# Optimization experiments

Measured on AMD Instinct MI355X. Metric: run time of the kernel, lower is better.

## Reference

```python
import jax, jax.numpy as jnp
import numpy as np

N = 50000       # num_nodes
R = 8           # num_relations
H = 64          # hidden_channels
C = 16          # num_classes
E = 1_600_000   # num edges (avg degree 32)
T = 8192        # number of 'author' target nodes (first T nodes after to_homogeneous)


def setup_inputs() -> dict:
    key = jax.random.key(0)
    ks = jax.random.split(key, 12)
    s = 0.02
    return {
        "edge_index": jax.random.randint(ks[0], (2, E), 0, N),
        "edge_type": jax.random.randint(ks[1], (E,), 0, R),
        "num_target": T,
        # conv1 (featureless: weight is an embedding table [R, N, H], root is [N, H])
        "weight1": jax.random.normal(ks[2], (R, N, H), jnp.float32) * s,
        "root1": jax.random.normal(ks[3], (N, H), jnp.float32) * s,
        "bias1": jnp.zeros((H,), jnp.float32),
        # conv2
        "weight2": jax.random.normal(ks[4], (R, H, H), jnp.float32) * s,
        "root2": jax.random.normal(ks[5], (H, H), jnp.float32) * s,
        "bias2": jnp.zeros((H,), jnp.float32),
        # linear head
        "lin_w": jax.random.normal(ks[6], (H, C), jnp.float32) * s,
        "lin_b": jnp.zeros((C,), jnp.float32),
    }


def reference(edge_index, edge_type, num_target, weight1, root1, bias1,
              weight2, root2, bias2, lin_w, lin_b):
    src, dst = edge_index[0], edge_index[1]
    E_ = src.shape[0]

    # PyG RGCNConv aggregates with MEAN per relation, then sums over relations.
    # Count edges per (dst node, relation) to form the per-relation mean denominator.
    seg = dst * R + edge_type                          # [E] combined (node, relation) id
    cnt = jax.ops.segment_sum(jnp.ones((E_,), jnp.float32), seg, num_segments=N * R)
    scale = (1.0 / jnp.maximum(cnt, 1.0))[seg]         # [E]

    # ---- conv1: x is None -> message = weight1[edge_type][src] (embedding lookup) ----
    m1 = weight1[edge_type, src] * scale[:, None]      # [E, H]
    h1 = jax.ops.segment_sum(m1, dst, num_segments=N)  # [N, H]
    h1 = h1 + root1 + bias1                            # root1[arange(N)] == root1
    h1 = jax.nn.elu(h1)

    # ---- conv2: message = h1[src] @ weight2[edge_type] ----
    # Precompute per-relation node transforms [R, N, H], then gather per edge.
    hr = jnp.einsum('nh,rhk->rnk', h1, weight2)        # [R, N, H]
    m2 = hr[edge_type, src] * scale[:, None]           # [E, H]
    h2 = jax.ops.segment_sum(m2, dst, num_segments=N)  # [N, H]
    h2 = h2 + h1 @ root2 + bias2
    h2 = jax.nn.elu(h2)

    # ---- linear head on the target ('author') node slice ----
    out = h2[:num_target] @ lin_w + lin_b              # [T, C]
    return out
```

## Files before the change

### kernel.cpp

```cpp
#include <hip/hip_runtime.h>

#define NNODES 50000
#define NREL   8
#define HID    64
#define NCLS   16
#define NEDGE  1600000
#define NTGT   8192
#define HALF   4096
#define NBINS  (NNODES * NREL)
#define CHUNK  1024
#define NCHUNK ((NBINS + CHUNK - 1) / CHUNK)

__device__ __forceinline__ float elu1(float x) { return x > 0.f ? x : expm1f(x); }

__device__ __forceinline__ int pack_rec(int src, int rel, int cnt) {
  return src | (rel << 16) | (cnt << 19);
}

__device__ __forceinline__ unsigned long long ld_stat(unsigned long long* p) {
  return __hip_atomic_load(p, __ATOMIC_RELAXED, __HIP_MEMORY_SCOPE_AGENT);
}
__device__ __forceinline__ void st_stat(unsigned long long* p, unsigned long long v) {
  __hip_atomic_store(p, v, __ATOMIC_RELAXED, __HIP_MEMORY_SCOPE_AGENT);
}

__global__ void count_kernel(const int* __restrict__ ei, const int* __restrict__ et,
                             int* __restrict__ cnt, int* __restrict__ epos,
                             unsigned long long* __restrict__ status) {
  int gt = blockIdx.x * blockDim.x + threadIdx.x;
  if (gt < NCHUNK) status[gt] = 0;
  int e4 = gt * 4;
  if (e4 >= NEDGE) return;
  int4 d = *(const int4*)(ei + NEDGE + e4);
  int4 r = *(const int4*)(et + e4);
  int4 p;
  p.x = atomicAdd(&cnt[d.x * NREL + r.x], 1);
  p.y = atomicAdd(&cnt[d.y * NREL + r.y], 1);
  p.z = atomicAdd(&cnt[d.z * NREL + r.z], 1);
  p.w = atomicAdd(&cnt[d.w * NREL + r.w], 1);
  *(int4*)(epos + e4) = p;
}

__global__ __launch_bounds__(256) void scan_lb_kernel(
    const int* __restrict__ cnt, unsigned long long* __restrict__ status,
    int* __restrict__ binptr) {
  __shared__ int sw[4];
  __shared__ int srun;
  __shared__ int sbase;
  int t = threadIdx.x, lane = t & 63, wid = t >> 6;
  int c = blockIdx.x;
  int i = c * CHUNK + t * 4;
  int4 cv = make_int4(0, 0, 0, 0);
  if (i < NBINS) cv = *(const int4*)(cnt + i);
  int p0 = cv.x, p1 = p0 + cv.y, p2 = p1 + cv.z, s = p2 + cv.w;
  int v = s;
#pragma unroll
  for (int off = 1; off < 64; off <<= 1) {
    int u = __shfl_up(v, off);
    if (lane >= off) v += u;
  }
  if (lane == 63) sw[wid] = v;
  __syncthreads();
  if (t == 0) {
    int run = 0;
#pragma unroll
    for (int j = 0; j < 4; ++j) { int x = sw[j]; sw[j] = run; run += x; }
    srun = run;
    unsigned long long f = (c == 0) ? 2ull : 1ull;
    st_stat(&status[c], (f << 62) | (unsigned)run);
    if (c == 0) sbase = 0;
  }
  __syncthreads();
  if (c > 0 && t < 64) {
    long long tot = 0;
    int back = c - 1;
    for (;;) {
      int idx = back - lane;
      unsigned long long st = (2ull << 62);
      if (idx >= 0) st = ld_stat(&status[idx]);
      int flag = (int)(st >> 62);
      bool isinc = (idx < 0) || (flag == 2);
      bool isval = (idx < 0) || (flag >= 1);
      unsigned long long incb = __ballot(isinc);
      unsigned long long valb = __ballot(isval);
      unsigned long long notval = ~valb;
      int firstinv = notval ? (__ffsll((long long)notval) - 1) : 64;
      int firstinc = incb ? (__ffsll((long long)incb) - 1) : 64;
      if (firstinc < firstinv) {
        int val = (lane <= firstinc) ? (int)(st & 0xFFFFFFFFu) : 0;
#pragma unroll
        for (int off = 32; off >= 1; off >>= 1) val += __shfl_xor(val, off);
        tot += val;
        break;
      } else if (firstinv > 0) {
        int val = (lane < firstinv) ? (int)(st & 0xFFFFFFFFu) : 0;
#pragma unroll
        for (int off = 32; off >= 1; off >>= 1) val += __shfl_xor(val, off);
        tot += val;
        back -= firstinv;
      } else {
        __builtin_amdgcn_s_sleep(2);
      }
    }
    if (lane == 0) {
      sbase = (int)tot;
      st_stat(&status[c], (2ull << 62) | (unsigned)((int)tot + srun));
    }
  }
  __syncthreads();
  int base = sbase;
  if (i < NBINS) {
    int excl = base + sw[wid] + (v - s);
    *(int4*)(binptr + i) = make_int4(excl, excl + p0, excl + p1, excl + p2);
  }
  if (c == 0 && t == 0) binptr[NBINS] = NEDGE;
}

__global__ void scatter_kernel(const int* __restrict__ ei, const int* __restrict__ et,
                               const int* __restrict__ epos, const int* __restrict__ binptr,
                               int* __restrict__ epo) {
  int e4 = (blockIdx.x * blockDim.x + threadIdx.x) * 4;
  if (e4 >= NEDGE) return;
  int4 sv = *(const int4*)(ei + e4);
  int4 dv = *(const int4*)(ei + NEDGE + e4);
  int4 rv = *(const int4*)(et + e4);
  int4 pv = *(const int4*)(epos + e4);
  int srcs[4] = {sv.x, sv.y, sv.z, sv.w};
  int dsts[4] = {dv.x, dv.y, dv.z, dv.w};
  int rels[4] = {rv.x, rv.y, rv.z, rv.w};
  int poss[4] = {pv.x, pv.y, pv.z, pv.w};
#pragma unroll
  for (int j = 0; j < 4; ++j) {
    int bin = dsts[j] * NREL + rels[j];
    int b = binptr[bin];
    int c = binptr[bin + 1] - b;
    epo[b + poss[j]] = pack_rec(srcs[j], rels[j], c);
  }
}

__global__ __launch_bounds__(256) void conv1_kernel(
    const int* __restrict__ binptr, const int* __restrict__ epo,
    const float* __restrict__ w1, const float* __restrict__ root1,
    const float* __restrict__ bias1, float* __restrict__ h1) {
  int wave = blockIdx.x * 4 + (threadIdx.x >> 6);
  if (wave >= NNODES) return;
  int lane = threadIdx.x & 63;
  int g = lane >> 4;
  int col = (lane & 15) << 2;
  int b0 = binptr[wave * NREL], b8 = binptr[wave * NREL + NREL];
  float4 acc = make_float4(0.f, 0.f, 0.f, 0.f);
  for (int eb = b0; eb < b8; eb += 64) {
    int mb = min(64, b8 - eb);
    int q = epo[eb + min(lane, mb - 1)];
    for (int j = 0; j < mb; j += 32) {
      float4 a[8]; float sc[8];
#pragma unroll
      for (int u = 0; u < 8; ++u) {
        int e0 = j + u * 4;
        if (e0 < mb) {
          int ei = e0 + g;
          int eic = min(ei, mb - 1);
          int rec = __shfl(q, eic);
          int src = rec & 0xFFFF;
          int rel = (rec >> 16) & 7;
          int cnt = ((unsigned)rec) >> 19;
          float s = 1.0f / (float)cnt;
          sc[u] = (ei < mb) ? s : 0.f;
          a[u] = *(const float4*)(w1 + (((size_t)(unsigned)(rel * NNODES + src)) << 6) + col);
        } else {
          sc[u] = 0.f;
          a[u] = make_float4(0.f, 0.f, 0.f, 0.f);
        }
      }
#pragma unroll
      for (int u = 0; u < 8; ++u) {
        acc.x = fmaf(a[u].x, sc[u], acc.x);
        acc.y = fmaf(a[u].y, sc[u], acc.y);
        acc.z = fmaf(a[u].z, sc[u], acc.z);
        acc.w = fmaf(a[u].w, sc[u], acc.w);
      }
    }
  }
#pragma unroll
  for (int off = 16; off < 64; off <<= 1) {
    acc.x += __shfl_xor(acc.x, off);
    acc.y += __shfl_xor(acc.y, off);
    acc.z += __shfl_xor(acc.z, off);
    acc.w += __shfl_xor(acc.w, off);
  }
  if (g == 0) {
    float4 r = *(const float4*)(root1 + (((size_t)wave) << 6) + col);
    float4 bz = *(const float4*)(bias1 + col);
    float4 v;
    v.x = elu1(acc.x + r.x + bz.x);
    v.y = elu1(acc.y + r.y + bz.y);
    v.z = elu1(acc.z + r.z + bz.z);
    v.w = elu1(acc.w + r.w + bz.w);
    *(float4*)(h1 + (((size_t)wave) << 6) + col) = v;
  }
}

__global__ __launch_bounds__(256) void conv2a_kernel(
    const int* __restrict__ binptr, const int* __restrict__ epo,
    const float* __restrict__ h1, float* __restrict__ agg, int nodeBase, int nloc) {
  int wv = blockIdx.x * 4 + (threadIdx.x >> 6);
  if (wv >= nloc * NREL) return;
  int lane = threadIdx.x & 63;
  int g = lane >> 4;
  int col = (lane & 15) << 2;
  int r = wv & 7;
  int bin = (nodeBase + (wv >> 3)) * NREL + r;
  int bb = binptr[bin], ee = binptr[bin + 1];
  float4 s = make_float4(0.f, 0.f, 0.f, 0.f);
  for (int e = bb; e < ee; e += 64) {
    int mb = min(64, ee - e);
    int q = epo[e + min(lane, mb - 1)];
    for (int j = 0; j < mb; j += 16) {
      float4 a[4]; float vld[4];
#pragma unroll
      for (int u = 0; u < 4; ++u) {
        int e0 = j + u * 4;
        if (e0 < mb) {
          int ei = e0 + g;
          int eic = min(ei, mb - 1);
          int src = __shfl(q, eic) & 0xFFFF;
          vld[u] = (ei < mb) ? 1.f : 0.f;
          a[u] = *(const float4*)(h1 + (((size_t)(unsigned)src) << 6) + col);
        } else {
          vld[u] = 0.f;
          a[u] = make_float4(0.f, 0.f, 0.f, 0.f);
        }
      }
#pragma unroll
      for (int u = 0; u < 4; ++u) {
        s.x = fmaf(a[u].x, vld[u], s.x);
        s.y = fmaf(a[u].y, vld[u], s.y);
        s.z = fmaf(a[u].z, vld[u], s.z);
        s.w = fmaf(a[u].w, vld[u], s.w);
      }
    }
  }
#pragma unroll
  for (int off = 16; off < 64; off <<= 1) {
    s.x += __shfl_xor(s.x, off);
    s.y += __shfl_xor(s.y, off);
    s.z += __shfl_xor(s.z, off);
    s.w += __shfl_xor(s.w, off);
  }
  if (g == 0) {
    float scl = (ee > bb) ? 1.0f / (float)(ee - bb) : 0.f;
    *(float4*)(agg + (((size_t)wv) << 6) + col) =
        make_float4(s.x * scl, s.y * scl, s.z * scl, s.w * scl);
  }
}

__global__ __launch_bounds__(256, 4) void conv2b_kernel(
    const float* __restrict__ agg, const float* __restrict__ h1,
    const float* __restrict__ w2, const float* __restrict__ root2,
    const float* __restrict__ bias2, const float* __restrict__ lin_w,
    const float* __restrict__ lin_b, float* __restrict__ out, int nodeBase) {
  __shared__ float sW[HID * HID];
  int t = threadIdx.x, lane = t & 63, wid = t >> 6;
  int ln0 = blockIdx.x * 8 + wid * 2;
  float bz = bias2[lane];
  float o0 = bz, o1 = bz;
  for (int r = 0; r < NREL; ++r) {
    if (r) __syncthreads();
#pragma unroll
    for (int i = 0; i < 4; ++i)
      *(float4*)(sW + t * 4 + i * 1024) = *(const float4*)(w2 + (r << 12) + t * 4 + i * 1024);
    __syncthreads();
    const float* a0 = agg + (((size_t)((ln0 + 0) * NREL + r)) << 6);
    const float* a1 = agg + (((size_t)((ln0 + 1) * NREL + r)) << 6);
#pragma unroll 16
    for (int k = 0; k < HID; ++k) {
      float w = sW[(k << 6) + lane];
      o0 = fmaf(a0[k], w, o0);
      o1 = fmaf(a1[k], w, o1);
    }
  }
  __syncthreads();
#pragma unroll
  for (int i = 0; i < 4; ++i)
    *(float4*)(sW + t * 4 + i * 1024) = *(const float4*)(root2 + t * 4 + i * 1024);
  __syncthreads();
  int g0 = nodeBase + ln0;
  const float* r0p = h1 + ((size_t)(g0 + 0) << 6);
  const float* r1p = h1 + ((size_t)(g0 + 1) << 6);
#pragma unroll 16
  for (int k = 0; k < HID; ++k) {
    float w = sW[(k << 6) + lane];
    o0 = fmaf(r0p[k], w, o0);
    o1 = fmaf(r1p[k], w, o1);
  }
  __syncthreads();
  int row0 = wid * 2;
  sW[row0 * 65 + lane] = elu1(o0);
  sW[(row0 + 1) * 65 + lane] = elu1(o1);
  float* lw = sW + 8 * 65;
  *(float4*)(lw + t * 4) = *(const float4*)(lin_w + t * 4);
  __syncthreads();
  if (t < 8 * NCLS) {
    int n = t >> 4, c = t & 15;
    float accv = lin_b[c];
#pragma unroll 16
    for (int l = 0; l < HID; ++l)
      accv = fmaf(sW[n * 65 + l], lw[l * NCLS + c], accv);
    out[((size_t)(nodeBase + blockIdx.x * 8 + n)) * NCLS + c] = accv;
  }
}

extern "C" void kernel_launch(void* const* d_in, const int* in_sizes, int n_in,
                              void* d_out, int out_size, void* d_ws, size_t ws_size,
                              hipStream_t stream) {
  const int*   ei    = (const int*)d_in[0];
  const int*   et    = (const int*)d_in[1];
  const float* w1    = (const float*)d_in[3];
  const float* root1 = (const float*)d_in[4];
  const float* bias1 = (const float*)d_in[5];
  const float* w2    = (const float*)d_in[6];
  const float* root2 = (const float*)d_in[7];
  const float* bias2 = (const float*)d_in[8];
  const float* lin_w = (const float*)d_in[9];
  const float* lin_b = (const float*)d_in[10];
  float* out = (float*)d_out;

  char* ws = (char*)d_ws;
  float* h1     = (float*)ws;
  int*   cnt    = (int*)ws;
  int*   epos   = (int*)(ws + (size_t)NBINS * 4);
  char*  p      = ws + (size_t)NNODES * HID * 4;
  int*   binptr = (int*)p;  p += ((size_t)(NBINS + 1) * 4 + 255) & ~(size_t)255;
  unsigned long long* status = (unsigned long long*)p;
  p += ((size_t)NCHUNK * 8 + 255) & ~(size_t)255;
  int*   epo    = (int*)p;  p += (size_t)NEDGE * 4;
  float* agg    = (float*)p;

  hipMemsetAsync(cnt, 0, (size_t)NBINS * sizeof(int), stream);
  count_kernel<<<(NEDGE / 4 + 255) / 256, 256, 0, stream>>>(ei, et, cnt, epos, status);
  scan_lb_kernel<<<NCHUNK, 256, 0, stream>>>(cnt, status, binptr);
  scatter_kernel<<<(NEDGE / 4 + 255) / 256, 256, 0, stream>>>(ei, et, epos, binptr, epo);
  conv1_kernel<<<(NNODES + 3) / 4, 256, 0, stream>>>(binptr, epo, w1, root1, bias1, h1);
  for (int c = 0; c < 2; ++c) {
    conv2a_kernel<<<(HALF * NREL) / 4, 256, 0, stream>>>(binptr, epo, h1, agg, c * HALF, HALF);
    conv2b_kernel<<<HALF / 8, 256, 0, stream>>>(agg, h1, w2, root2, bias2, lin_w, lin_b,
                                                out, c * HALF);
  }
}
```

Measured before the change: 406.9 us.

## Drop per-edge position buffer by atomically bumping bin offsets during scatter

The count pass no longer records each edge's slot within its bin. Instead, scatter atomically increments the exclusive bin offsets, which leaves binptr holding inclusive end offsets, and the conv kernels now read bin bounds as binptr[bin-1] and binptr[bin]. This saves the 1.6M-int epos write and read, at the cost of atomics with return values in scatter and a nondeterministic edge order inside each bin. The conv2 launch also processes all targets in one chunk when the workspace is large enough, halving the conv2 launches.

```diff
diff --git a/kernel.cpp b/kernel.cpp
--- a/kernel.cpp
+++ b/kernel.cpp
@@ -25,7 +25,7 @@
 }
 
 __global__ void count_kernel(const int* __restrict__ ei, const int* __restrict__ et,
-                             int* __restrict__ cnt, int* __restrict__ epos,
+                             int* __restrict__ cnt,
                              unsigned long long* __restrict__ status) {
   int gt = blockIdx.x * blockDim.x + threadIdx.x;
   if (gt < NCHUNK) status[gt] = 0;
@@ -33,12 +33,10 @@
   if (e4 >= NEDGE) return;
   int4 d = *(const int4*)(ei + NEDGE + e4);
   int4 r = *(const int4*)(et + e4);
-  int4 p;
-  p.x = atomicAdd(&cnt[d.x * NREL + r.x], 1);
-  p.y = atomicAdd(&cnt[d.y * NREL + r.y], 1);
-  p.z = atomicAdd(&cnt[d.z * NREL + r.z], 1);
-  p.w = atomicAdd(&cnt[d.w * NREL + r.w], 1);
-  *(int4*)(epos + e4) = p;
+  atomicAdd(&cnt[d.x * NREL + r.x], 1);
+  atomicAdd(&cnt[d.y * NREL + r.y], 1);
+  atomicAdd(&cnt[d.z * NREL + r.z], 1);
+  atomicAdd(&cnt[d.w * NREL + r.w], 1);
 }
 
 __global__ __launch_bounds__(256) void scan_lb_kernel(
@@ -117,24 +115,22 @@
 }
 
 __global__ void scatter_kernel(const int* __restrict__ ei, const int* __restrict__ et,
-                               const int* __restrict__ epos, const int* __restrict__ binptr,
+                               const int* __restrict__ cnt, int* __restrict__ binptr,
                                int* __restrict__ epo) {
   int e4 = (blockIdx.x * blockDim.x + threadIdx.x) * 4;
   if (e4 >= NEDGE) return;
   int4 sv = *(const int4*)(ei + e4);
   int4 dv = *(const int4*)(ei + NEDGE + e4);
   int4 rv = *(const int4*)(et + e4);
-  int4 pv = *(const int4*)(epos + e4);
   int srcs[4] = {sv.x, sv.y, sv.z, sv.w};
   int dsts[4] = {dv.x, dv.y, dv.z, dv.w};
   int rels[4] = {rv.x, rv.y, rv.z, rv.w};
-  int poss[4] = {pv.x, pv.y, pv.z, pv.w};
 #pragma unroll
   for (int j = 0; j < 4; ++j) {
     int bin = dsts[j] * NREL + rels[j];
-    int b = binptr[bin];
-    int c = binptr[bin + 1] - b;
-    epo[b + poss[j]] = pack_rec(srcs[j], rels[j], c);
+    int pos = atomicAdd(&binptr[bin], 1);
+    int c = cnt[bin];
+    epo[pos] = pack_rec(srcs[j], rels[j], c);
   }
 }
 
@@ -147,7 +143,9 @@
   int lane = threadIdx.x & 63;
   int g = lane >> 4;
   int col = (lane & 15) << 2;
-  int b0 = binptr[wave * NREL], b8 = binptr[wave * NREL + NREL];
+  int base = wave * NREL;
+  int b0 = (wave == 0) ? 0 : binptr[base - 1];
+  int b8 = binptr[base + 7];
   float4 acc = make_float4(0.f, 0.f, 0.f, 0.f);
   for (int eb = b0; eb < b8; eb += 64) {
     int mb = min(64, b8 - eb);
@@ -210,7 +208,8 @@
   int col = (lane & 15) << 2;
   int r = wv & 7;
   int bin = (nodeBase + (wv >> 3)) * NREL + r;
-  int bb = binptr[bin], ee = binptr[bin + 1];
+  int bb = (bin == 0) ? 0 : binptr[bin - 1];
+  int ee = binptr[bin];
   float4 s = make_float4(0.f, 0.f, 0.f, 0.f);
   for (int e = bb; e < ee; e += 64) {
     int mb = min(64, ee - e);
@@ -328,22 +327,23 @@
   char* ws = (char*)d_ws;
   float* h1     = (float*)ws;
   int*   cnt    = (int*)ws;
-  int*   epos   = (int*)(ws + (size_t)NBINS * 4);
   char*  p      = ws + (size_t)NNODES * HID * 4;
   int*   binptr = (int*)p;  p += ((size_t)(NBINS + 1) * 4 + 255) & ~(size_t)255;
   unsigned long long* status = (unsigned long long*)p;
   p += ((size_t)NCHUNK * 8 + 255) & ~(size_t)255;
   int*   epo    = (int*)p;  p += (size_t)NEDGE * 4;
   float* agg    = (float*)p;
+  size_t fixed  = (size_t)(p - ws);
+  int chunk = (fixed + (size_t)NTGT * NREL * HID * 4 <= ws_size) ? NTGT : HALF;
 
   hipMemsetAsync(cnt, 0, (size_t)NBINS * sizeof(int), stream);
-  count_kernel<<<(NEDGE / 4 + 255) / 256, 256, 0, stream>>>(ei, et, cnt, epos, status);
+  count_kernel<<<(NEDGE / 4 + 255) / 256, 256, 0, stream>>>(ei, et, cnt, status);
   scan_lb_kernel<<<NCHUNK, 256, 0, stream>>>(cnt, status, binptr);
-  scatter_kernel<<<(NEDGE / 4 + 255) / 256, 256, 0, stream>>>(ei, et, epos, binptr, epo);
+  scatter_kernel<<<(NEDGE / 4 + 255) / 256, 256, 0, stream>>>(ei, et, cnt, binptr, epo);
   conv1_kernel<<<(NNODES + 3) / 4, 256, 0, stream>>>(binptr, epo, w1, root1, bias1, h1);
-  for (int c = 0; c < 2; ++c) {
-    conv2a_kernel<<<(HALF * NREL) / 4, 256, 0, stream>>>(binptr, epo, h1, agg, c * HALF, HALF);
-    conv2b_kernel<<<HALF / 8, 256, 0, stream>>>(agg, h1, w2, root2, bias2, lin_w, lin_b,
-                                                out, c * HALF);
-  }
-}
+  for (int c = 0; c < NTGT / chunk; ++c) {
+    conv2a_kernel<<<(chunk * NREL) / 4, 256, 0, stream>>>(binptr, epo, h1, agg, c * chunk, chunk);
+    conv2b_kernel<<<chunk / 8, 256, 0, stream>>>(agg, h1, w2, root2, bias2, lin_w, lin_b,
+                                                 out, c * chunk);
+  }
+}
```

New measurement: 432.7 us. 1.06x slower.

## Aggregate all relations per node in one wave and process targets in one chunk

Applied to the files above, without the earlier changes.

conv2a now assigns one wave per destination node instead of one wave per (node, relation) bin. It walks all of the node's edges together and routes each message into one of eight per-relation accumulators, using the packed relation and count fields for the mean scale. This removes the short per-bin loops that left lanes idle at average degree 4 per bin, and it drops the per-bin binptr reads. In exchange it spends eight FMAs per edge element on masked routing and needs many more registers for the accumulators. The host also launches a single chunk covering all target nodes when the workspace is large enough, which halves the conv2a/conv2b launch pairs.

```diff
diff --git a/kernel.cpp b/kernel.cpp
--- a/kernel.cpp
+++ b/kernel.cpp
@@ -204,53 +204,64 @@
     const int* __restrict__ binptr, const int* __restrict__ epo,
     const float* __restrict__ h1, float* __restrict__ agg, int nodeBase, int nloc) {
   int wv = blockIdx.x * 4 + (threadIdx.x >> 6);
-  if (wv >= nloc * NREL) return;
+  if (wv >= nloc) return;
   int lane = threadIdx.x & 63;
   int g = lane >> 4;
   int col = (lane & 15) << 2;
-  int r = wv & 7;
-  int bin = (nodeBase + (wv >> 3)) * NREL + r;
-  int bb = binptr[bin], ee = binptr[bin + 1];
-  float4 s = make_float4(0.f, 0.f, 0.f, 0.f);
-  for (int e = bb; e < ee; e += 64) {
-    int mb = min(64, ee - e);
-    int q = epo[e + min(lane, mb - 1)];
-    for (int j = 0; j < mb; j += 16) {
-      float4 a[4]; float vld[4];
-#pragma unroll
-      for (int u = 0; u < 4; ++u) {
+  int node = nodeBase + wv;
+  int b0 = binptr[node * NREL], b8 = binptr[node * NREL + NREL];
+  float4 acc[NREL];
+#pragma unroll
+  for (int r = 0; r < NREL; ++r) acc[r] = make_float4(0.f, 0.f, 0.f, 0.f);
+  for (int eb = b0; eb < b8; eb += 64) {
+    int mb = min(64, b8 - eb);
+    int q = epo[eb + min(lane, mb - 1)];
+    for (int j = 0; j < mb; j += 32) {
+      float4 a[8]; float sc[8]; int rl[8];
+#pragma unroll
+      for (int u = 0; u < 8; ++u) {
         int e0 = j + u * 4;
         if (e0 < mb) {
           int ei = e0 + g;
           int eic = min(ei, mb - 1);
-          int src = __shfl(q, eic) & 0xFFFF;
-          vld[u] = (ei < mb) ? 1.f : 0.f;
+          int rec = __shfl(q, eic);
+          int src = rec & 0xFFFF;
+          rl[u] = (rec >> 16) & 7;
+          int cnt = ((unsigned)rec) >> 19;
+          sc[u] = (ei < mb) ? 1.0f / (float)cnt : 0.f;
           a[u] = *(const float4*)(h1 + (((size_t)(unsigned)src) << 6) + col);
         } else {
-          vld[u] = 0.f;
+          sc[u] = 0.f; rl[u] = 0;
           a[u] = make_float4(0.f, 0.f, 0.f, 0.f);
         }
       }
 #pragma unroll
-      for (int u = 0; u < 4; ++u) {
-        s.x = fmaf(a[u].x, vld[u], s.x);
-        s.y = fmaf(a[u].y, vld[u], s.y);
-        s.z = fmaf(a[u].z, vld[u], s.z);
-        s.w = fmaf(a[u].w, vld[u], s.w);
-      }
-    }
-  }
-#pragma unroll
-  for (int off = 16; off < 64; off <<= 1) {
-    s.x += __shfl_xor(s.x, off);
-    s.y += __shfl_xor(s.y, off);
-    s.z += __shfl_xor(s.z, off);
-    s.w += __shfl_xor(s.w, off);
+      for (int u = 0; u < 8; ++u) {
+#pragma unroll
+        for (int r = 0; r < NREL; ++r) {
+          float m = (rl[u] == r) ? sc[u] : 0.f;
+          acc[r].x = fmaf(a[u].x, m, acc[r].x);
+          acc[r].y = fmaf(a[u].y, m, acc[r].y);
+          acc[r].z = fmaf(a[u].z, m, acc[r].z);
+          acc[r].w = fmaf(a[u].w, m, acc[r].w);
+        }
+      }
+    }
+  }
+#pragma unroll
+  for (int r = 0; r < NREL; ++r) {
+#pragma unroll
+    for (int off = 16; off < 64; off <<= 1) {
+      acc[r].x += __shfl_xor(acc[r].x, off);
+      acc[r].y += __shfl_xor(acc[r].y, off);
+      acc[r].z += __shfl_xor(acc[r].z, off);
+      acc[r].w += __shfl_xor(acc[r].w, off);
+    }
   }
   if (g == 0) {
-    float scl = (ee > bb) ? 1.0f / (float)(ee - bb) : 0.f;
-    *(float4*)(agg + (((size_t)wv) << 6) + col) =
-        make_float4(s.x * scl, s.y * scl, s.z * scl, s.w * scl);
+#pragma unroll
+    for (int r = 0; r < NREL; ++r)
+      *(float4*)(agg + (((size_t)(wv * NREL + r)) << 6) + col) = acc[r];
   }
 }
 
@@ -335,15 +346,17 @@
   p += ((size_t)NCHUNK * 8 + 255) & ~(size_t)255;
   int*   epo    = (int*)p;  p += (size_t)NEDGE * 4;
   float* agg    = (float*)p;
+  size_t fixed  = (size_t)(p - ws);
+  int chunk = (fixed + (size_t)NTGT * NREL * HID * 4 <= ws_size) ? NTGT : HALF;
 
   hipMemsetAsync(cnt, 0, (size_t)NBINS * sizeof(int), stream);
   count_kernel<<<(NEDGE / 4 + 255) / 256, 256, 0, stream>>>(ei, et, cnt, epos, status);
   scan_lb_kernel<<<NCHUNK, 256, 0, stream>>>(cnt, status, binptr);
   scatter_kernel<<<(NEDGE / 4 + 255) / 256, 256, 0, stream>>>(ei, et, epos, binptr, epo);
   conv1_kernel<<<(NNODES + 3) / 4, 256, 0, stream>>>(binptr, epo, w1, root1, bias1, h1);
-  for (int c = 0; c < 2; ++c) {
-    conv2a_kernel<<<(HALF * NREL) / 4, 256, 0, stream>>>(binptr, epo, h1, agg, c * HALF, HALF);
-    conv2b_kernel<<<HALF / 8, 256, 0, stream>>>(agg, h1, w2, root2, bias2, lin_w, lin_b,
-                                                out, c * HALF);
-  }
-}
+  for (int c = 0; c < NTGT / chunk; ++c) {
+    conv2a_kernel<<<(chunk + 3) / 4, 256, 0, stream>>>(binptr, epo, h1, agg, c * chunk, chunk);
+    conv2b_kernel<<<chunk / 8, 256, 0, stream>>>(agg, h1, w2, root2, bias2, lin_w, lin_b,
+                                                 out, c * chunk);
+  }
+}
```

New measurement: 401.2 us. Within noise of the previous version (-1.4%).
